# Optimization experiments

Hardware: AMD Instinct MI355X
Metric: run time of the kernel (lower is better)

## Reference

```python
import jax, jax.numpy as jnp
import numpy as np
from jax import lax

HID = 96              # hidden_dim (C)
DM  = 2 * HID         # SS2D d_model (real+imag interleaved channels)
DI  = 2 * DM          # d_inner (expand=2, VMamba default)
N   = 16              # d_state
K   = 4               # scan directions
R   = (DM + 15) // 16 # dt_rank = ceil(d_model/16)
B_, H_, W_ = 1, 64, 64


def _layernorm(x, w, b, eps=1e-5):
    m = x.mean(-1, keepdims=True)
    v = ((x - m) ** 2).mean(-1, keepdims=True)
    return (x - m) * lax.rsqrt(v + eps) * w + b


def _selective_scan(xs, delta, A, Bs, Cs):
    # xs, delta: (B,K,D,L); A: (K,D,N); Bs, Cs: (B,K,N,L)
    def step(h, inp):
        dt, Bt, Ct, ut = inp                              # (B,K,D),(B,K,N),(B,K,N),(B,K,D)
        dA = jnp.exp(dt[..., None] * A[None])             # (B,K,D,N)
        h = h * dA + dt[..., None] * Bt[:, :, None, :] * ut[..., None]
        y = jnp.einsum('bkdn,bkn->bkd', h, Ct)
        return h, y
    inputs = (jnp.moveaxis(delta, -1, 0), jnp.moveaxis(Bs, -1, 0),
              jnp.moveaxis(Cs, -1, 0), jnp.moveaxis(xs, -1, 0))
    h0 = jnp.zeros(xs.shape[:3] + (N,), xs.dtype)
    _, ys = lax.scan(step, h0, inputs)                    # (L,B,K,D)
    return jnp.moveaxis(ys, 0, -1)                        # (B,K,D,L)


def _forward_core(x, x_proj_w, dt_w, dt_b, A_logs, Ds):
    # x: (B, DI, H, W) -- 4-direction cross-scan (VMamba SS2D)
    B, D, H, W = x.shape
    L = H * W
    x_hw = x.reshape(B, D, L)
    x_wh = x.transpose(0, 1, 3, 2).reshape(B, D, L)
    x_hwwh = jnp.stack([x_hw, x_wh], axis=1)                    # (B,2,D,L)
    xs = jnp.concatenate([x_hwwh, jnp.flip(x_hwwh, -1)], 1)     # (B,4,D,L)
    x_dbl = jnp.einsum('bkdl,kcd->bkcl', xs, x_proj_w)          # (B,K,R+2N,L)
    dts, Bs, Cs = jnp.split(x_dbl, [R, R + N], axis=2)
    dts = jnp.einsum('bkrl,kdr->bkdl', dts, dt_w)
    delta = jax.nn.softplus(dts + dt_b[None, :, :, None])
    A = -jnp.exp(A_logs.reshape(K, D, N))
    ys = _selective_scan(xs, delta, A, Bs, Cs)
    out_y = ys + Ds.reshape(K, D)[None, :, :, None] * xs        # (B,4,D,L)
    inv_y = jnp.flip(out_y[:, 2:4], -1)
    tr = lambda t: t.reshape(B, D, W, H).transpose(0, 1, 3, 2).reshape(B, D, L)
    y = out_y[:, 0] + inv_y[:, 0] + tr(out_y[:, 1]) + tr(inv_y[:, 1])
    return y.transpose(0, 2, 1).reshape(B, H, W, D)


def _ss2d(x, in_proj_w, conv_w, conv_b, x_proj_w, dt_w, dt_b,
          A_logs, Ds, out_norm_w, out_norm_b, out_proj_w):
    # x: (B, H, Wf, DM)
    xz = x @ in_proj_w.T                                        # (B,H,Wf,2*DI)
    xc, z = jnp.split(xz, 2, axis=-1)
    xc = xc.transpose(0, 3, 1, 2)                               # (B,DI,H,Wf)
    xc = lax.conv_general_dilated(xc, conv_w, (1, 1), 'SAME',
                                  feature_group_count=DI,
                                  dimension_numbers=('NCHW', 'OIHW', 'NCHW'))
    xc = jax.nn.silu(xc + conv_b[None, :, None, None])
    y = _forward_core(xc, x_proj_w, dt_w, dt_b, A_logs, Ds)     # (B,H,Wf,DI)
    y = _layernorm(y, out_norm_w, out_norm_b)
    y = y * jax.nn.silu(z)
    return y @ out_proj_w.T                                     # (B,H,Wf,DM)


def _freq_vss(x, in_proj_w, conv_w, conv_b, x_proj_w, dt_w, dt_b,
              A_logs, Ds, out_norm_w, out_norm_b, out_proj_w):
    B, H, W, C = x.shape
    xf = jnp.fft.rfft2(x, axes=(1, 2), norm='ortho')            # (B,H,Wf,C) complex
    Wf = xf.shape[2]
    # interleave real/imag into channels: (B,H,Wf,C,2) -> (B,H,Wf,2C)
    x1 = jnp.stack([xf.real, xf.imag], axis=4).reshape(B, H, Wf, 2 * C)
    att = _ss2d(x1, in_proj_w, conv_w, conv_b, x_proj_w, dt_w, dt_b,
                A_logs, Ds, out_norm_w, out_norm_b, out_proj_w)
    att = att.reshape(B, H, Wf, C, 2)
    attc = lax.complex(att[..., 0], att[..., 1])
    x1r = jnp.fft.irfft2(attc, s=(H, W), axes=(1, 2), norm='ortho')
    return x + x1r                                              # residual (drop_path=0)


def setup_inputs() -> dict:
    key = jax.random.key(0)
    ks = jax.random.split(key, 8)
    s = 0.02
    return {
        'x': jax.random.normal(ks[0], (B_, H_, W_, HID), jnp.float32),
        'in_proj_w': jax.random.normal(ks[1], (2 * DI, DM), jnp.float32) * s,
        'conv_w': jax.random.normal(ks[2], (DI, 1, 3, 3), jnp.float32) * s,
        'conv_b': jnp.zeros((DI,), jnp.float32),
        'x_proj_w': jax.random.normal(ks[3], (K, R + 2 * N, DI), jnp.float32) * s,
        'dt_w': jax.random.normal(ks[4], (K, DI, R), jnp.float32) * s,
        'dt_b': jax.random.normal(ks[5], (K, DI), jnp.float32) * 0.1,
        'A_logs': jnp.tile(jnp.log(jnp.arange(1, N + 1, dtype=jnp.float32))[None], (K * DI, 1)),
        'Ds': jnp.ones((K * DI,), jnp.float32),
        'out_norm_w': jnp.ones((DI,), jnp.float32),
        'out_norm_b': jnp.zeros((DI,), jnp.float32),
        'out_proj_w': jax.random.normal(ks[6], (DM, DI), jnp.float32) * s,
    }


def reference(x, in_proj_w, conv_w, conv_b, x_proj_w, dt_w, dt_b,
              A_logs, Ds, out_norm_w, out_norm_b, out_proj_w):
    return _freq_vss(x, in_proj_w, conv_w, conv_b, x_proj_w, dt_w, dt_b,
                     A_logs, Ds, out_norm_w, out_norm_b, out_proj_w)
```

## Files before the change

kernel.cpp:

```cpp
#include <hip/hip_runtime.h>
#include <hip/hip_bf16.h>

#define LQ   2112
#define DQ   384
#define NST  16
#define HQ   64
#define WFQ  33
#define CQ   96
#define SC   66
#define KDN  24576

#define AIPW  0
#define ACW   147456
#define ACB   150912
#define AXPW  151296
#define ADTW  218880
#define ADTB  237312
#define AANEG 238848
#define ADS   263424
#define ANW   264960
#define ANB   265344
#define AOPW  265728
#define ARTOT 339456

#define OFF_FFT   339456
#define OFF_XZ    744960
#define OFF_XCV   2366976
#define OFF_G     3177984
#define OFF_SUMDT 3549696
#define OFF_HEND  3651072
#define OFF_YS    5273088

#define P_ZR  0
#define P_ZI  202752

static __device__ __forceinline__ float u2f(unsigned short u)
{ union { unsigned int i; float f; } v; v.i = ((unsigned int)u) << 16; return v.f; }

static __device__ __forceinline__ float ldin(const void* p, int o, int isbf)
{
    if (isbf) return u2f(((const unsigned short*)p)[o]);
    return ((const float*)p)[o];
}

static __device__ __forceinline__ int isbf_of(const void* ds)
{ return (((const unsigned int*)ds)[0] == 0x3F803F80u) ? 1 : 0; }

__global__ __launch_bounds__(256) void k_cvt_rfftw(
    const void* __restrict__ x,   const void* __restrict__ ipw,
    const void* __restrict__ cw,  const void* __restrict__ cb,
    const void* __restrict__ xpw, const void* __restrict__ dtw,
    const void* __restrict__ dtb, const void* __restrict__ alog,
    const void* __restrict__ ds,  const void* __restrict__ nw,
    const void* __restrict__ nb,  const void* __restrict__ opw,
    float* __restrict__ arena, float* __restrict__ Zr, float* __restrict__ Zi)
{
    const int isbf = isbf_of(ds);
    if (blockIdx.x < 1326) {
        int t = blockIdx.x * 256 + threadIdx.x;
        int o = t;
        if (o < 147456) { arena[t] = ldin(ipw, o, isbf); return; }  o -= 147456;
        if (o < 3456)   { arena[t] = ldin(cw, o, isbf);  return; }  o -= 3456;
        if (o < 384)    { arena[t] = ldin(cb, o, isbf);  return; }  o -= 384;
        if (o < 67584)  { arena[t] = ldin(xpw, o, isbf); return; }  o -= 67584;
        if (o < 18432)  { arena[t] = ldin(dtw, o, isbf); return; }  o -= 18432;
        if (o < 1536)   { arena[t] = ldin(dtb, o, isbf); return; }  o -= 1536;
        if (o < 24576)  { arena[t] = -expf(ldin(alog, o, isbf)); return; }  o -= 24576;
        if (o < 1536)   { arena[t] = ldin(ds, o, isbf);  return; }  o -= 1536;
        if (o < 384)    { arena[t] = ldin(nw, o, isbf);  return; }  o -= 384;
        if (o < 384)    { arena[t] = ldin(nb, o, isbf);  return; }  o -= 384;
        arena[t] = ldin(opw, o, isbf);
        return;
    }
    __shared__ float tc[64], ts[64];
    if (threadIdx.x < 64) {
        float ang = -6.283185307179586f * (float)threadIdx.x / 64.f;
        float s, c; __sincosf(ang, &s, &c); tc[threadIdx.x] = c; ts[threadIdx.x] = s;
    }
    __syncthreads();
    int tid = (blockIdx.x - 1326) * 256 + threadIdx.x;
    int c = tid % CQ; int f = (tid / CQ) % WFQ; int h = tid / (CQ * WFQ);
    const int base = h * 64 * CQ + c;
    float zr = 0.f, zi = 0.f; int j = 0;
    for (int w = 0; w < 64; w++) {
        float xv = ldin(x, base + w * CQ, isbf);
        zr += xv * tc[j]; zi += xv * ts[j];
        j += f; j &= 63;
    }
    Zr[tid] = zr; Zi[tid] = zi;
}

__global__ __launch_bounds__(256) void k_ffth(const float* __restrict__ Zr, const float* __restrict__ Zi,
                                              float* __restrict__ x1)
{
    __shared__ float tc[64], ts[64];
    if (threadIdx.x < 64) {
        float ang = -6.283185307179586f * (float)threadIdx.x / 64.f;
        float s, c; __sincosf(ang, &s, &c); tc[threadIdx.x] = c; ts[threadIdx.x] = s;
    }
    __syncthreads();
    int tid = blockIdx.x * 256 + threadIdx.x;
    int c = tid % CQ; int f = (tid / CQ) % WFQ; int u = tid / (CQ * WFQ);
    float xr = 0.f, xi = 0.f; int j = 0;
    int base = f * CQ + c;
    for (int h = 0; h < 64; h++) {
        float zr = Zr[base + h * (WFQ * CQ)];
        float zi = Zi[base + h * (WFQ * CQ)];
        xr += zr * tc[j] - zi * ts[j];
        xi += zr * ts[j] + zi * tc[j];
        j += u; j &= 63;
    }
    int l = u * WFQ + f;
    x1[l * 192 + 2 * c]     = xr * (1.f / 64.f);
    x1[l * 192 + 2 * c + 1] = xi * (1.f / 64.f);
}

typedef __attribute__((ext_vector_type(8))) __bf16 bf16x8;
typedef __attribute__((ext_vector_type(4))) float f32x4;

__global__ __launch_bounds__(256) void k_gemm(const float* __restrict__ A, const float* __restrict__ W,
                                              float* __restrict__ C, int N, int K, int sW, int sC)
{
    W += (size_t)blockIdx.z * sW; C += (size_t)blockIdx.z * sC;
    __shared__ __bf16 Asm[64 * 40];
    __shared__ __bf16 Bsm[64 * 40];
    const int tid = threadIdx.x;
    const int bm = blockIdx.y * 64, bn = blockIdx.x * 64;
    const int wv = tid >> 6, lane = tid & 63;
    const int srow = tid >> 2, skk = (tid & 3) * 8;
    const int fm = lane & 15, fq = lane >> 4;
    f32x4 acc0 = {0.f, 0.f, 0.f, 0.f}, acc1 = acc0, acc2 = acc0, acc3 = acc0;
    const __bf16* afp = Asm + (wv * 16 + fm) * 40 + fq * 8;
    const __bf16* bfp = Bsm + fm * 40 + fq * 8;
    for (int k0 = 0; k0 < K; k0 += 32) {
        {
            const float* ap = A + (size_t)(bm + srow) * K + k0 + skk;
            float4 a0 = *(const float4*)ap, a1 = *(const float4*)(ap + 4);
            bf16x8 v = { (__bf16)a0.x, (__bf16)a0.y, (__bf16)a0.z, (__bf16)a0.w,
                         (__bf16)a1.x, (__bf16)a1.y, (__bf16)a1.z, (__bf16)a1.w };
            *(bf16x8*)(Asm + srow * 40 + skk) = v;
        }
        {
            float4 b0 = {0.f,0.f,0.f,0.f}, b1 = b0;
            if (bn + srow < N) {
                const float* wp = W + (size_t)(bn + srow) * K + k0 + skk;
                b0 = *(const float4*)wp; b1 = *(const float4*)(wp + 4);
            }
            bf16x8 v = { (__bf16)b0.x, (__bf16)b0.y, (__bf16)b0.z, (__bf16)b0.w,
                         (__bf16)b1.x, (__bf16)b1.y, (__bf16)b1.z, (__bf16)b1.w };
            *(bf16x8*)(Bsm + srow * 40 + skk) = v;
        }
        __syncthreads();
        bf16x8 af = *(const bf16x8*)afp;
        bf16x8 fb0 = *(const bf16x8*)(bfp);
        bf16x8 fb1 = *(const bf16x8*)(bfp + 16 * 40);
        bf16x8 fb2 = *(const bf16x8*)(bfp + 32 * 40);
        bf16x8 fb3 = *(const bf16x8*)(bfp + 48 * 40);
        acc0 = __builtin_amdgcn_mfma_f32_16x16x32_bf16(af, fb0, acc0, 0, 0, 0);
        acc1 = __builtin_amdgcn_mfma_f32_16x16x32_bf16(af, fb1, acc1, 0, 0, 0);
        acc2 = __builtin_amdgcn_mfma_f32_16x16x32_bf16(af, fb2, acc2, 0, 0, 0);
        acc3 = __builtin_amdgcn_mfma_f32_16x16x32_bf16(af, fb3, acc3, 0, 0, 0);
        __syncthreads();
    }
    const int m0 = bm + wv * 16 + fq * 4;
#pragma unroll
    for (int nt = 0; nt < 4; nt++) {
        f32x4 a = (nt == 0) ? acc0 : ((nt == 1) ? acc1 : ((nt == 2) ? acc2 : acc3));
        int n = bn + nt * 16 + fm;
        if (n < N) {
#pragma unroll
            for (int r = 0; r < 4; r++)
                C[(size_t)(m0 + r) * N + n] = a[r];
        }
    }
}

__global__ __launch_bounds__(256) void k_conv(const float* __restrict__ xz,
                                              const float* __restrict__ ar,
                                              float* __restrict__ xcv)
{
    int tid = blockIdx.x * 256 + threadIdx.x;
    int d = tid % DQ; int lp = tid / DQ;
    int l0 = lp * 2;
    float w9[9];
#pragma unroll
    for (int i = 0; i < 9; i++) w9[i] = ar[ACW + d * 9 + i];
    float cb = ar[ACB + d];
#pragma unroll
    for (int q = 0; q < 2; q++) {
        int l = l0 + q;
        int h = l / WFQ; int f = l % WFQ;
        float acc = cb;
#pragma unroll
        for (int ky = 0; ky < 3; ky++) {
            int hh = h + ky - 1;
            if (hh < 0 || hh >= HQ) continue;
#pragma unroll
            for (int kx = 0; kx < 3; kx++) {
                int ff = f + kx - 1;
                if (ff < 0 || ff >= WFQ) continue;
                acc += w9[ky * 3 + kx] * xz[(size_t)(hh * WFQ + ff) * 768 + d];
            }
        }
        float sig = 1.f / (1.f + __expf(-acc));
        xcv[(size_t)l * DQ + d] = acc * sig;
    }
}

static __device__ __forceinline__ float softplus_f(float a)
{
    return (a > 15.f) ? a : __logf(1.f + __expf(a));
}

template<int KK> static __device__ __forceinline__ int chunk_l0(int s)
{
    if (KK == 0) return s * 32;
    if (KK == 1) return (s & 1) * 1056 + (s >> 1);
    if (KK == 2) return 2111 - s * 32;
    return 2111 - (s & 1) * 1056 - (s >> 1);
}
template<int KK> static __device__ __forceinline__ int chunk_stp()
{
    if (KK == 0) return 1;
    if (KK == 1) return 33;
    if (KK == 2) return -1;
    return -33;
}

template<int KK, int PASS2> static __device__ __forceinline__ void scan_body(
    const float* __restrict__ xcv, const float* __restrict__ G, const float* __restrict__ ar,
    float* __restrict__ hend, float* __restrict__ sumdt, float* __restrict__ ysum,
    float* __restrict__ dtL, float* __restrict__ duL)
{
    const int s = blockIdx.x, db = blockIdx.y;
    const int lane = threadIdx.x;
    const int d = lane & 15, ng = lane >> 4;
    const int stp = chunk_stp<KK>();
    const int l0 = chunk_l0<KK>(s);
    const float* Gk = G + (size_t)KK * (LQ * 44);

    {
        const int st = lane & 31;
        const int jb = (lane >> 5) * 8;
        const int lt = l0 + stp * st;
        const float* gr = Gk + lt * 44;
        float4 g0 = *(const float4*)(gr);
        float4 g1 = *(const float4*)(gr + 4);
        float4 g2 = *(const float4*)(gr + 8);
        const float* ub = xcv + (size_t)lt * DQ + db * 16 + jb;
        float uu[8];
        *(float4*)(uu)     = *(const float4*)(ub);
        *(float4*)(uu + 4) = *(const float4*)(ub + 4);
#pragma unroll 4
        for (int j = 0; j < 8; j++) {
            const int kdj = KK * DQ + db * 16 + jb + j;
            const float* wp = ar + ADTW + kdj * 12;
            float acc = ar[ADTB + kdj]
                + wp[0] * g0.x + wp[1] * g0.y + wp[2]  * g0.z + wp[3]  * g0.w
                + wp[4] * g1.x + wp[5] * g1.y + wp[6]  * g1.z + wp[7]  * g1.w
                + wp[8] * g2.x + wp[9] * g2.y + wp[10] * g2.z + wp[11] * g2.w;
            float dtv = softplus_f(acc);
            dtL[st * 17 + jb + j] = dtv;
            duL[st * 17 + jb + j] = dtv * uu[j];
        }
    }
    if (!PASS2 && KK == 0 && lane < 32) {
        float4 z4 = make_float4(0.f, 0.f, 0.f, 0.f);
        float* zp = ysum + (size_t)(l0 + lane) * DQ + db * 16;
        *(float4*)zp = z4; *(float4*)(zp + 4) = z4;
        *(float4*)(zp + 8) = z4; *(float4*)(zp + 12) = z4;
    }
    __syncthreads();

    const int kd = KK * DQ + db * 16 + d;
    const int kdn = kd * NST + 4 * ng;
    const float4 Av = *(const float4*)(ar + AANEG + kdn);
    float h0 = 0.f, h1 = 0.f, h2 = 0.f, h3 = 0.f;
    if (PASS2) {
        float4 hh = *(const float4*)(hend + (size_t)s * KDN + kdn);
        h0 = hh.x; h1 = hh.y; h2 = hh.z; h3 = hh.w;
    }

#pragma unroll 8
    for (int i = 0; i < 32; i++) {
        const int l = l0 + stp * i;
        float dt = dtL[i * 17 + d];
        float du = duL[i * 17 + d];
        float4 bv = *(const float4*)(Gk + l * 44 + 12 + 4 * ng);
        h0 = h0 * __expf(dt * Av.x) + du * bv.x;
        h1 = h1 * __expf(dt * Av.y) + du * bv.y;
        h2 = h2 * __expf(dt * Av.z) + du * bv.z;
        h3 = h3 * __expf(dt * Av.w) + du * bv.w;
        if (PASS2) {
            float4 cv = *(const float4*)(Gk + l * 44 + 28 + 4 * ng);
            float yp = h0 * cv.x + h1 * cv.y + h2 * cv.z + h3 * cv.w;
            yp += __shfl_xor(yp, 16);
            yp += __shfl_xor(yp, 32);
            if (ng == 0) atomicAdd(&ysum[(size_t)l * DQ + db * 16 + d], yp);
        }
    }

    if (!PASS2) {
        *(float4*)(hend + (size_t)s * KDN + kdn) = make_float4(h0, h1, h2, h3);
        float sd = 0.f;
#pragma unroll
        for (int t = 0; t < 8; t++) sd += dtL[(ng * 8 + t) * 17 + d];
        sd += __shfl_xor(sd, 16);
        sd += __shfl_xor(sd, 32);
        if (ng == 0) sumdt[s * 1536 + kd] = sd;
    }
}

__global__ __launch_bounds__(64, 8) void k_scan1(const float* __restrict__ xcv, const float* __restrict__ G,
                                                 const float* __restrict__ ar,
                                                 float* __restrict__ hend, float* __restrict__ sumdt,
                                                 float* __restrict__ ysum)
{
    __shared__ float smem[2 * 32 * 17];
    float* dtL = smem; float* duL = smem + 32 * 17;
    switch (blockIdx.z) {
        case 0: scan_body<0, 0>(xcv, G, ar, hend, sumdt, ysum, dtL, duL); break;
        case 1: scan_body<1, 0>(xcv, G, ar, hend, sumdt, ysum, dtL, duL); break;
        case 2: scan_body<2, 0>(xcv, G, ar, hend, sumdt, ysum, dtL, duL); break;
        default: scan_body<3, 0>(xcv, G, ar, hend, sumdt, ysum, dtL, duL); break;
    }
}

__global__ __launch_bounds__(64, 8) void k_scan2(const float* __restrict__ xcv, const float* __restrict__ G,
                                                 const float* __restrict__ ar,
                                                 float* __restrict__ hend, float* __restrict__ sumdt,
                                                 float* __restrict__ ysum)
{
    __shared__ float smem[2 * 32 * 17];
    float* dtL = smem; float* duL = smem + 32 * 17;
    switch (blockIdx.z) {
        case 0: scan_body<0, 1>(xcv, G, ar, hend, sumdt, ysum, dtL, duL); break;
        case 1: scan_body<1, 1>(xcv, G, ar, hend, sumdt, ysum, dtL, duL); break;
        case 2: scan_body<2, 1>(xcv, G, ar, hend, sumdt, ysum, dtL, duL); break;
        default: scan_body<3, 1>(xcv, G, ar, hend, sumdt, ysum, dtL, duL); break;
    }
}

__global__ __launch_bounds__(256) void k_comb(const float* __restrict__ ar, const float* __restrict__ sumdt,
                                              float* __restrict__ hend)
{
    int tid = blockIdx.x * 256 + threadIdx.x;
    int kd = tid >> 4;
    float Av = ar[AANEG + tid];
    float hp = 0.f;
    for (int s = 0; s < SC; s++) {
        float he = hend[(size_t)s * KDN + tid];
        hend[(size_t)s * KDN + tid] = hp;
        hp = hp * __expf(Av * sumdt[s * 1536 + kd]) + he;
    }
}

__global__ __launch_bounds__(128) void k_lnmul(const float* __restrict__ ysum, const float* __restrict__ xcv,
                                               const float* __restrict__ xz, const float* __restrict__ ar,
                                               float* __restrict__ ym)
{
    int l = blockIdx.x; int tid = threadIdx.x;
    float v[3]; float s1 = 0.f, s2 = 0.f;
#pragma unroll
    for (int j = 0; j < 3; j++) {
        int d = tid + j * 128;
        size_t idx = (size_t)l * DQ + d;
        float sd = ar[ADS + d] + ar[ADS + DQ + d] + ar[ADS + 2 * DQ + d] + ar[ADS + 3 * DQ + d];
        float a = ysum[idx] + sd * xcv[idx];
        v[j] = a; s1 += a; s2 += a * a;
    }
#pragma unroll
    for (int off = 1; off < 64; off <<= 1) { s1 += __shfl_xor(s1, off); s2 += __shfl_xor(s2, off); }
    __shared__ float sh[4];
    if ((tid & 63) == 0) { sh[(tid >> 6) * 2] = s1; sh[(tid >> 6) * 2 + 1] = s2; }
    __syncthreads();
    s1 = sh[0] + sh[2]; s2 = sh[1] + sh[3];
    float m = s1 * (1.f / 384.f);
    float var = s2 * (1.f / 384.f) - m * m;
    float rs = rsqrtf(var + 1e-5f);
#pragma unroll
    for (int j = 0; j < 3; j++) {
        int d = tid + j * 128;
        float z = xz[(size_t)l * 768 + 384 + d];
        float sig = 1.f / (1.f + __expf(-z));
        ym[(size_t)l * DQ + d] = ((v[j] - m) * rs * ar[ANW + d] + ar[ANB + d]) * (z * sig);
    }
}

__global__ __launch_bounds__(256) void k_iffth(const float* __restrict__ att,
                                               float* __restrict__ Yr, float* __restrict__ Yi)
{
    __shared__ float tc[64], ts[64];
    if (threadIdx.x < 64) {
        float ang = 6.283185307179586f * (float)threadIdx.x / 64.f;
        float s, c; __sincosf(ang, &s, &c); tc[threadIdx.x] = c; ts[threadIdx.x] = s;
    }
    __syncthreads();
    int tid = blockIdx.x * 256 + threadIdx.x;
    int c = tid % CQ; int f = (tid / CQ) % WFQ; int hp = tid / (CQ * WFQ);
    float yr = 0.f, yi = 0.f; int j = 0;
    for (int h = 0; h < 64; h++) {
        const float* ap = att + (size_t)(h * WFQ + f) * 192 + 2 * c;
        float arv = ap[0], aiv = ap[1];
        yr += arv * tc[j] - aiv * ts[j];
        yi += arv * ts[j] + aiv * tc[j];
        j += hp; j &= 63;
    }
    Yr[tid] = yr * 0.125f;
    Yi[tid] = yi * 0.125f;
}

__global__ __launch_bounds__(256) void k_irfft_res(const float* __restrict__ Yr, const float* __restrict__ Yi,
                                                   const void* __restrict__ x, const void* __restrict__ ds,
                                                   void* __restrict__ out)
{
    __shared__ float tc[64], ts[64];
    if (threadIdx.x < 64) {
        float ang = 6.283185307179586f * (float)threadIdx.x / 64.f;
        float s, c; __sincosf(ang, &s, &c); tc[threadIdx.x] = c; ts[threadIdx.x] = s;
    }
    __syncthreads();
    const int isbf = isbf_of(ds);
    int tid = blockIdx.x * 256 + threadIdx.x;
    int c = tid % CQ; int w = (tid / CQ) % 64; int h = tid / (CQ * 64);
    const float* yr = Yr + h * (WFQ * CQ) + c;
    const float* yi = Yi + h * (WFQ * CQ) + c;
    float acc = yr[0];
    acc += ((w & 1) ? -1.f : 1.f) * yr[32 * CQ];
    float a2 = 0.f; int j = w & 63;
    for (int f = 1; f < 32; f++) {
        a2 += yr[f * CQ] * tc[j] - yi[f * CQ] * ts[j];
        j += w; j &= 63;
    }
    acc += 2.f * a2;
    float val = ldin(x, tid, isbf) + 0.125f * acc;
    if (isbf) ((__hip_bfloat16*)out)[tid] = __float2bfloat16(val);
    else      ((float*)out)[tid] = val;
}

extern "C" void kernel_launch(void* const* d_in, const int* in_sizes, int n_in,
                              void* d_out, int out_size, void* d_ws, size_t ws_size,
                              hipStream_t stream)
{
    float* ws    = (float*)d_ws;
    float* ar    = ws;
    float* Zr    = ws + OFF_FFT + P_ZR;
    float* Zi    = ws + OFF_FFT + P_ZI;
    float* xz    = ws + OFF_XZ;
    float* xcv   = ws + OFF_XCV;
    float* G     = ws + OFF_G;
    float* sumdt = ws + OFF_SUMDT;
    float* hend  = ws + OFF_HEND;
    float* YS    = ws + OFF_YS;

    float* x1   = YS;
    float* ysum = YS;
    float* ym   = hend;
    float* att  = xcv;

    k_cvt_rfftw<<<2118, 256, 0, stream>>>(d_in[0], d_in[1], d_in[2], d_in[3], d_in[4], d_in[5],
                                          d_in[6], d_in[7], d_in[8], d_in[9], d_in[10], d_in[11],
                                          ar, Zr, Zi);
    k_ffth<<<792, 256, 0, stream>>>(Zr, Zi, x1);
    k_gemm<<<dim3(12, 33, 1), 256, 0, stream>>>(x1, ar + AIPW, xz, 768, 192, 0, 0);
    k_conv<<<1584, 256, 0, stream>>>(xz, ar, xcv);
    k_gemm<<<dim3(1, 33, 4), 256, 0, stream>>>(xcv, ar + AXPW, G, 44, 384, 44 * 384, LQ * 44);
    k_scan1<<<dim3(SC, 24, 4), 64, 0, stream>>>(xcv, G, ar, hend, sumdt, ysum);
    k_comb<<<96, 256, 0, stream>>>(ar, sumdt, hend);
    k_scan2<<<dim3(SC, 24, 4), 64, 0, stream>>>(xcv, G, ar, hend, sumdt, ysum);
    k_lnmul<<<LQ, 128, 0, stream>>>(ysum, xcv, xz, ar, ym);
    k_gemm<<<dim3(3, 33, 1), 256, 0, stream>>>(ym, ar + AOPW, att, 192, 384, 0, 0);
    k_iffth<<<792, 256, 0, stream>>>(att, Zr, Zi);
    k_irfft_res<<<1536, 256, 0, stream>>>(Zr, Zi, d_in[0], d_in[8], d_out);
}
```

Before: 225.0 us.

## Fuse LayerNorm gating into out_proj GEMM, lengthen scan chunks, unroll DFT loops

Replaces the separate LayerNorm/SiLU-gate kernel and the following generic GEMM with one kernel. It computes per-row statistics, builds normalized gated bf16 tiles in shared memory and multiplies them with MFMA. This removes the intermediate ym round trip and one launch. The chunked selective scan now uses 33 chunks of 64 steps instead of 66 of 32, which halves the hidden-state and cross-chunk combine traffic but lengthens each block's serial recurrence and lowers occupancy bounds. Several DFT loops also receive unroll-by-4 pragmas.

```diff
diff --git a/kernel.cpp b/kernel.cpp
--- a/kernel.cpp
+++ b/kernel.cpp
@@ -7,7 +7,7 @@
 #define HQ   64
 #define WFQ  33
 #define CQ   96
-#define SC   66
+#define SC   33
 #define KDN  24576
 
 #define AIPW  0
@@ -82,6 +82,7 @@
     int c = tid % CQ; int f = (tid / CQ) % WFQ; int h = tid / (CQ * WFQ);
     const int base = h * 64 * CQ + c;
     float zr = 0.f, zi = 0.f; int j = 0;
+#pragma unroll 4
     for (int w = 0; w < 64; w++) {
         float xv = ldin(x, base + w * CQ, isbf);
         zr += xv * tc[j]; zi += xv * ts[j];
@@ -103,6 +104,7 @@
     int c = tid % CQ; int f = (tid / CQ) % WFQ; int u = tid / (CQ * WFQ);
     float xr = 0.f, xi = 0.f; int j = 0;
     int base = f * CQ + c;
+#pragma unroll 4
     for (int h = 0; h < 64; h++) {
         float zr = Zr[base + h * (WFQ * CQ)];
         float zi = Zi[base + h * (WFQ * CQ)];
@@ -214,10 +216,10 @@
 
 template<int KK> static __device__ __forceinline__ int chunk_l0(int s)
 {
-    if (KK == 0) return s * 32;
-    if (KK == 1) return (s & 1) * 1056 + (s >> 1);
-    if (KK == 2) return 2111 - s * 32;
-    return 2111 - (s & 1) * 1056 - (s >> 1);
+    if (KK == 0) return s * 64;
+    if (KK == 1) return s;
+    if (KK == 2) return 2111 - s * 64;
+    return 2111 - s;
 }
 template<int KK> static __device__ __forceinline__ int chunk_stp()
 {
@@ -240,31 +242,32 @@
     const float* Gk = G + (size_t)KK * (LQ * 44);
 
     {
-        const int st = lane & 31;
-        const int jb = (lane >> 5) * 8;
+        const int st = lane;
         const int lt = l0 + stp * st;
         const float* gr = Gk + lt * 44;
         float4 g0 = *(const float4*)(gr);
         float4 g1 = *(const float4*)(gr + 4);
         float4 g2 = *(const float4*)(gr + 8);
-        const float* ub = xcv + (size_t)lt * DQ + db * 16 + jb;
-        float uu[8];
-        *(float4*)(uu)     = *(const float4*)(ub);
-        *(float4*)(uu + 4) = *(const float4*)(ub + 4);
-#pragma unroll 4
-        for (int j = 0; j < 8; j++) {
-            const int kdj = KK * DQ + db * 16 + jb + j;
+        const float* ub = xcv + (size_t)lt * DQ + db * 16;
+        float uu[16];
+        *(float4*)(uu)      = *(const float4*)(ub);
+        *(float4*)(uu + 4)  = *(const float4*)(ub + 4);
+        *(float4*)(uu + 8)  = *(const float4*)(ub + 8);
+        *(float4*)(uu + 12) = *(const float4*)(ub + 12);
+#pragma unroll
+        for (int j = 0; j < 16; j++) {
+            const int kdj = KK * DQ + db * 16 + j;
             const float* wp = ar + ADTW + kdj * 12;
             float acc = ar[ADTB + kdj]
                 + wp[0] * g0.x + wp[1] * g0.y + wp[2]  * g0.z + wp[3]  * g0.w
                 + wp[4] * g1.x + wp[5] * g1.y + wp[6]  * g1.z + wp[7]  * g1.w
                 + wp[8] * g2.x + wp[9] * g2.y + wp[10] * g2.z + wp[11] * g2.w;
             float dtv = softplus_f(acc);
-            dtL[st * 17 + jb + j] = dtv;
-            duL[st * 17 + jb + j] = dtv * uu[j];
-        }
-    }
-    if (!PASS2 && KK == 0 && lane < 32) {
+            dtL[st * 17 + j] = dtv;
+            duL[st * 17 + j] = dtv * uu[j];
+        }
+    }
+    if (!PASS2 && KK == 0) {
         float4 z4 = make_float4(0.f, 0.f, 0.f, 0.f);
         float* zp = ysum + (size_t)(l0 + lane) * DQ + db * 16;
         *(float4*)zp = z4; *(float4*)(zp + 4) = z4;
@@ -282,7 +285,7 @@
     }
 
 #pragma unroll 8
-    for (int i = 0; i < 32; i++) {
+    for (int i = 0; i < 64; i++) {
         const int l = l0 + stp * i;
         float dt = dtL[i * 17 + d];
         float du = duL[i * 17 + d];
@@ -304,20 +307,20 @@
         *(float4*)(hend + (size_t)s * KDN + kdn) = make_float4(h0, h1, h2, h3);
         float sd = 0.f;
 #pragma unroll
-        for (int t = 0; t < 8; t++) sd += dtL[(ng * 8 + t) * 17 + d];
+        for (int t = 0; t < 16; t++) sd += dtL[(ng * 16 + t) * 17 + d];
         sd += __shfl_xor(sd, 16);
         sd += __shfl_xor(sd, 32);
         if (ng == 0) sumdt[s * 1536 + kd] = sd;
     }
 }
 
-__global__ __launch_bounds__(64, 8) void k_scan1(const float* __restrict__ xcv, const float* __restrict__ G,
+__global__ __launch_bounds__(64, 4) void k_scan1(const float* __restrict__ xcv, const float* __restrict__ G,
                                                  const float* __restrict__ ar,
                                                  float* __restrict__ hend, float* __restrict__ sumdt,
                                                  float* __restrict__ ysum)
 {
-    __shared__ float smem[2 * 32 * 17];
-    float* dtL = smem; float* duL = smem + 32 * 17;
+    __shared__ float smem[2 * 64 * 17];
+    float* dtL = smem; float* duL = smem + 64 * 17;
     switch (blockIdx.z) {
         case 0: scan_body<0, 0>(xcv, G, ar, hend, sumdt, ysum, dtL, duL); break;
         case 1: scan_body<1, 0>(xcv, G, ar, hend, sumdt, ysum, dtL, duL); break;
@@ -326,13 +329,13 @@
     }
 }
 
-__global__ __launch_bounds__(64, 8) void k_scan2(const float* __restrict__ xcv, const float* __restrict__ G,
+__global__ __launch_bounds__(64, 4) void k_scan2(const float* __restrict__ xcv, const float* __restrict__ G,
                                                  const float* __restrict__ ar,
                                                  float* __restrict__ hend, float* __restrict__ sumdt,
                                                  float* __restrict__ ysum)
 {
-    __shared__ float smem[2 * 32 * 17];
-    float* dtL = smem; float* duL = smem + 32 * 17;
+    __shared__ float smem[2 * 64 * 17];
+    float* dtL = smem; float* duL = smem + 64 * 17;
     switch (blockIdx.z) {
         case 0: scan_body<0, 1>(xcv, G, ar, hend, sumdt, ysum, dtL, duL); break;
         case 1: scan_body<1, 1>(xcv, G, ar, hend, sumdt, ysum, dtL, duL); break;
@@ -355,35 +358,106 @@
     }
 }
 
-__global__ __launch_bounds__(128) void k_lnmul(const float* __restrict__ ysum, const float* __restrict__ xcv,
-                                               const float* __restrict__ xz, const float* __restrict__ ar,
-                                               float* __restrict__ ym)
-{
-    int l = blockIdx.x; int tid = threadIdx.x;
-    float v[3]; float s1 = 0.f, s2 = 0.f;
-#pragma unroll
-    for (int j = 0; j < 3; j++) {
-        int d = tid + j * 128;
-        size_t idx = (size_t)l * DQ + d;
-        float sd = ar[ADS + d] + ar[ADS + DQ + d] + ar[ADS + 2 * DQ + d] + ar[ADS + 3 * DQ + d];
-        float a = ysum[idx] + sd * xcv[idx];
-        v[j] = a; s1 += a; s2 += a * a;
-    }
-#pragma unroll
-    for (int off = 1; off < 64; off <<= 1) { s1 += __shfl_xor(s1, off); s2 += __shfl_xor(s2, off); }
-    __shared__ float sh[4];
-    if ((tid & 63) == 0) { sh[(tid >> 6) * 2] = s1; sh[(tid >> 6) * 2 + 1] = s2; }
-    __syncthreads();
-    s1 = sh[0] + sh[2]; s2 = sh[1] + sh[3];
-    float m = s1 * (1.f / 384.f);
-    float var = s2 * (1.f / 384.f) - m * m;
-    float rs = rsqrtf(var + 1e-5f);
-#pragma unroll
-    for (int j = 0; j < 3; j++) {
-        int d = tid + j * 128;
-        float z = xz[(size_t)l * 768 + 384 + d];
-        float sig = 1.f / (1.f + __expf(-z));
-        ym[(size_t)l * DQ + d] = ((v[j] - m) * rs * ar[ANW + d] + ar[ANB + d]) * (z * sig);
+__global__ __launch_bounds__(256) void k_lngemm(const float* __restrict__ ysum, const float* __restrict__ xcv,
+                                                const float* __restrict__ xz, const float* __restrict__ ar,
+                                                float* __restrict__ att)
+{
+    __shared__ __bf16 Asm[64 * 40];
+    __shared__ __bf16 Bsm[64 * 40];
+    __shared__ float rowm[64], rowr[64];
+    __shared__ float sdk[DQ], nwk[DQ], nbk[DQ];
+    const int tid = threadIdx.x;
+    const int bm = blockIdx.y * 64, bn = blockIdx.x * 64;
+
+    for (int k = tid; k < DQ; k += 256) {
+        sdk[k] = ar[ADS + k] + ar[ADS + DQ + k] + ar[ADS + 2 * DQ + k] + ar[ADS + 3 * DQ + k];
+        nwk[k] = ar[ANW + k];
+        nbk[k] = ar[ANB + k];
+    }
+    __syncthreads();
+
+    {
+        const int r = tid >> 2, seg = tid & 3;
+        const float* yp = ysum + (size_t)(bm + r) * DQ + seg * 96;
+        const float* xp = xcv  + (size_t)(bm + r) * DQ + seg * 96;
+        float s1 = 0.f, s2 = 0.f;
+#pragma unroll 8
+        for (int k = 0; k < 96; k += 4) {
+            float4 yv = *(const float4*)(yp + k);
+            float4 xv = *(const float4*)(xp + k);
+            float4 sv = *(const float4*)(sdk + seg * 96 + k);
+            float a0 = yv.x + sv.x * xv.x; float a1 = yv.y + sv.y * xv.y;
+            float a2 = yv.z + sv.z * xv.z; float a3 = yv.w + sv.w * xv.w;
+            s1 += a0 + a1 + a2 + a3;
+            s2 += a0 * a0 + a1 * a1 + a2 * a2 + a3 * a3;
+        }
+        s1 += __shfl_xor(s1, 1); s2 += __shfl_xor(s2, 1);
+        s1 += __shfl_xor(s1, 2); s2 += __shfl_xor(s2, 2);
+        if (seg == 0) {
+            float m = s1 * (1.f / 384.f);
+            float var = s2 * (1.f / 384.f) - m * m;
+            rowm[r] = m; rowr[r] = rsqrtf(var + 1e-5f);
+        }
+    }
+    __syncthreads();
+
+    const int wv = tid >> 6, lane = tid & 63;
+    const int srow = tid >> 2, skk = (tid & 3) * 8;
+    const int fm = lane & 15, fq = lane >> 4;
+    f32x4 acc0 = {0.f, 0.f, 0.f, 0.f}, acc1 = acc0, acc2 = acc0, acc3 = acc0;
+    const __bf16* afp = Asm + (wv * 16 + fm) * 40 + fq * 8;
+    const __bf16* bfp = Bsm + fm * 40 + fq * 8;
+    const float W_rm = rowm[srow], W_rr = rowr[srow];
+    for (int k0 = 0; k0 < 384; k0 += 32) {
+        {
+            const size_t rb = (size_t)(bm + srow) * DQ + k0 + skk;
+            float4 y0 = *(const float4*)(ysum + rb), y1 = *(const float4*)(ysum + rb + 4);
+            float4 x0 = *(const float4*)(xcv + rb),  x1 = *(const float4*)(xcv + rb + 4);
+            const float* zp = xz + (size_t)(bm + srow) * 768 + 384 + k0 + skk;
+            float4 z0 = *(const float4*)(zp), z1 = *(const float4*)(zp + 4);
+            float va[8];
+            float ya[8] = { y0.x, y0.y, y0.z, y0.w, y1.x, y1.y, y1.z, y1.w };
+            float xa[8] = { x0.x, x0.y, x0.z, x0.w, x1.x, x1.y, x1.z, x1.w };
+            float za[8] = { z0.x, z0.y, z0.z, z0.w, z1.x, z1.y, z1.z, z1.w };
+#pragma unroll
+            for (int e = 0; e < 8; e++) {
+                int k = k0 + skk + e;
+                float a = ya[e] + sdk[k] * xa[e];
+                float zn = za[e];
+                float sig = 1.f / (1.f + __expf(-zn));
+                va[e] = ((a - W_rm) * W_rr * nwk[k] + nbk[k]) * (zn * sig);
+            }
+            bf16x8 v = { (__bf16)va[0], (__bf16)va[1], (__bf16)va[2], (__bf16)va[3],
+                         (__bf16)va[4], (__bf16)va[5], (__bf16)va[6], (__bf16)va[7] };
+            *(bf16x8*)(Asm + srow * 40 + skk) = v;
+        }
+        {
+            const float* wp = ar + AOPW + (size_t)(bn + srow) * 384 + k0 + skk;
+            float4 b0 = *(const float4*)wp, b1 = *(const float4*)(wp + 4);
+            bf16x8 v = { (__bf16)b0.x, (__bf16)b0.y, (__bf16)b0.z, (__bf16)b0.w,
+                         (__bf16)b1.x, (__bf16)b1.y, (__bf16)b1.z, (__bf16)b1.w };
+            *(bf16x8*)(Bsm + srow * 40 + skk) = v;
+        }
+        __syncthreads();
+        bf16x8 af = *(const bf16x8*)afp;
+        bf16x8 fb0 = *(const bf16x8*)(bfp);
+        bf16x8 fb1 = *(const bf16x8*)(bfp + 16 * 40);
+        bf16x8 fb2 = *(const bf16x8*)(bfp + 32 * 40);
+        bf16x8 fb3 = *(const bf16x8*)(bfp + 48 * 40);
+        acc0 = __builtin_amdgcn_mfma_f32_16x16x32_bf16(af, fb0, acc0, 0, 0, 0);
+        acc1 = __builtin_amdgcn_mfma_f32_16x16x32_bf16(af, fb1, acc1, 0, 0, 0);
+        acc2 = __builtin_amdgcn_mfma_f32_16x16x32_bf16(af, fb2, acc2, 0, 0, 0);
+        acc3 = __builtin_amdgcn_mfma_f32_16x16x32_bf16(af, fb3, acc3, 0, 0, 0);
+        __syncthreads();
+    }
+    const int m0 = bm + wv * 16 + fq * 4;
+#pragma unroll
+    for (int nt = 0; nt < 4; nt++) {
+        f32x4 a = (nt == 0) ? acc0 : ((nt == 1) ? acc1 : ((nt == 2) ? acc2 : acc3));
+        int n = bn + nt * 16 + fm;
+#pragma unroll
+        for (int r = 0; r < 4; r++)
+            att[(size_t)(m0 + r) * 192 + n] = a[r];
     }
 }
 
@@ -399,6 +473,7 @@
     int tid = blockIdx.x * 256 + threadIdx.x;
     int c = tid % CQ; int f = (tid / CQ) % WFQ; int hp = tid / (CQ * WFQ);
     float yr = 0.f, yi = 0.f; int j = 0;
+#pragma unroll 4
     for (int h = 0; h < 64; h++) {
         const float* ap = att + (size_t)(h * WFQ + f) * 192 + 2 * c;
         float arv = ap[0], aiv = ap[1];
@@ -428,6 +503,7 @@
     float acc = yr[0];
     acc += ((w & 1) ? -1.f : 1.f) * yr[32 * CQ];
     float a2 = 0.f; int j = w & 63;
+#pragma unroll 4
     for (int f = 1; f < 32; f++) {
         a2 += yr[f * CQ] * tc[j] - yi[f * CQ] * ts[j];
         j += w; j &= 63;
@@ -455,8 +531,7 @@
 
     float* x1   = YS;
     float* ysum = YS;
-    float* ym   = hend;
-    float* att  = xcv;
+    float* att  = hend;
 
     k_cvt_rfftw<<<2118, 256, 0, stream>>>(d_in[0], d_in[1], d_in[2], d_in[3], d_in[4], d_in[5],
                                           d_in[6], d_in[7], d_in[8], d_in[9], d_in[10], d_in[11],
@@ -468,8 +543,7 @@
     k_scan1<<<dim3(SC, 24, 4), 64, 0, stream>>>(xcv, G, ar, hend, sumdt, ysum);
     k_comb<<<96, 256, 0, stream>>>(ar, sumdt, hend);
     k_scan2<<<dim3(SC, 24, 4), 64, 0, stream>>>(xcv, G, ar, hend, sumdt, ysum);
-    k_lnmul<<<LQ, 128, 0, stream>>>(ysum, xcv, xz, ar, ym);
-    k_gemm<<<dim3(3, 33, 1), 256, 0, stream>>>(ym, ar + AOPW, att, 192, 384, 0, 0);
+    k_lngemm<<<dim3(3, 33, 1), 256, 0, stream>>>(ysum, xcv, xz, ar, att);
     k_iffth<<<792, 256, 0, stream>>>(att, Zr, Zi);
     k_irfft_res<<<1536, 256, 0, stream>>>(Zr, Zi, d_in[0], d_in[8], d_out);
 }
```

New measurement: 226.7 us. About the same (+0.8%).
